# Performance work log

Measured on AMD Instinct MI355X. Metric: run time of the kernel, lower is better.

The kernel has to match this reference:

```python
import jax, jax.numpy as jnp
import numpy as np

B, C, H, W = 4, 256, 64, 64

def _conv1x1(x, w, b):
    # x: [B,C,H,W], w: [O,C] (1x1 conv kernel squeezed), b: [O]
    return jnp.einsum('bchw,oc->bohw', x, w) + b[None, :, None, None]

def setup_inputs() -> dict:
    key = jax.random.key(0)
    ks = jax.random.split(key, 9)
    s = 1.0 / np.sqrt(C)
    inp = {'x': jax.random.normal(ks[0], (B, C, H, W), dtype=jnp.float32)}
    for i, name in enumerate(['f', 'g', 'h', 'v']):
        inp['W' + name] = jax.random.uniform(ks[1 + 2 * i], (C, C), jnp.float32, -s, s)
        inp['b' + name] = jax.random.uniform(ks[2 + 2 * i], (C,), jnp.float32, -s, s)
    return inp

def reference(x, Wf, bf, Wg, bg, Wh, bh, Wv, bv):
    b, c, h, w = x.shape
    n = h * w
    f = _conv1x1(x, Wf, bf).reshape(b, c, n)  # [B,C,N]
    g = _conv1x1(x, Wg, bg).reshape(b, c, n)  # [B,C,N]
    hh = _conv1x1(x, Wh, bh).reshape(b, c, n)  # [B,C,N]
    fg = jnp.einsum('bci,bcj->bij', f, g)      # [B,N,N], no scaling (as in source)
    attn = jax.nn.softmax(fg, axis=1)          # softmax over dim=1 (first N axis)
    fgh = jnp.einsum('bci,bij->bcj', hh, attn) # [B,C,N]
    return _conv1x1(fgh.reshape(b, c, h, w), Wv, bv)
```

## Files before the change

kernel.cpp:

```cpp
#include <hip/hip_runtime.h>
#include <hip/hip_bf16.h>


typedef short short8 __attribute__((ext_vector_type(8)));
typedef short short4v __attribute__((ext_vector_type(4)));
typedef float f32x4 __attribute__((ext_vector_type(4)));
typedef _Float16 f16x8 __attribute__((ext_vector_type(8)));
typedef unsigned short u16;
typedef unsigned int u32;

#define DEV static __device__ __forceinline__
#define MFMA16(a, b, c) __builtin_amdgcn_mfma_f32_16x16x32_f16(a, b, c, 0, 0, 0)

DEV u16 h16(float x) {
    union { _Float16 h; u16 u; } c;
    c.h = (_Float16)x;
    return c.u;
}
DEV f16x8 ldh8(const u16* p) { return *reinterpret_cast<const f16x8*>(p); }

DEV u32 cvtpk(float a, float b) {
    u32 r;
    asm("v_cvt_pkrtz_f16_f32 %0, %1, %2" : "=v"(r) : "v"(a), "v"(b));
    return r;
}

DEV void gload16(const void* g, void* l) {
    __builtin_amdgcn_global_load_lds(
        (const __attribute__((address_space(1))) unsigned int*)g,
        (__attribute__((address_space(3))) unsigned int*)l, 16, 0, 0);
}

constexpr size_t OFF_WH = 0;
constexpr size_t OFF_WV = 131072;
constexpr size_t OFF_MB = 262144;
constexpr size_t OFF_ML = 266240;
constexpr size_t OFF_M  = 524288;
constexpr size_t OFF_U  = 1310720;
constexpr size_t OFF_H  = OFF_U + 8388608;
constexpr size_t OFF_XT = OFF_H + 8388608;
constexpr size_t OFF_OP = OFF_XT + 8388608;

__global__ __launch_bounds__(256) void k_gemm_M(
    const float* __restrict__ Wf, const float* __restrict__ Wg,
    const float* __restrict__ bg, const float* __restrict__ Wh,
    const float* __restrict__ Wv,
    u16* __restrict__ M, float* __restrict__ Mb, u16* WH, u16* WV) {
    int c = blockIdx.x;
    int t = threadIdx.x;
    size_t rowi = (size_t)c * 256 + t;
    WH[rowi] = h16(Wh[rowi]);
    WV[rowi] = h16(Wv[rowi]);
    __shared__ float wf[256];
    wf[t] = Wf[(size_t)t * 256 + c];
    __syncthreads();
    float acc = 0.f;
    for (int o = 0; o < 256; ++o) acc += wf[o] * Wg[(size_t)o * 256 + t];
    M[rowi] = h16(acc);
    if (t == 0) {
        float s = 0.f;
        for (int o = 0; o < 256; ++o) s += wf[o] * bg[o];
        Mb[c] = s;
    }
}

__global__ __launch_bounds__(256) void k_prep(
    const float* __restrict__ x, const u16* __restrict__ M,
    const float* __restrict__ Mb, const u16* __restrict__ WH,
    const float* __restrict__ bh,
    u16* __restrict__ Xt, u16* __restrict__ U, u16* __restrict__ Hb) {
    __shared__ float tbuf[64][65];
    __shared__ u16 xt[64][264];

    int bid = blockIdx.x;
    int m0 = bid * 64;
    int b = m0 >> 12, n0 = m0 & 4095;
    int tid = threadIdx.x;
    int tx = tid & 63, ty = tid >> 6;
    int nl = tid >> 2, cg = tid & 3;

    for (int ct4 = 0; ct4 < 4; ++ct4) {
        const float* src = x + ((size_t)(b * 256 + ct4 * 64)) * 4096 + n0;
#pragma unroll
        for (int k = 0; k < 16; ++k) {
            int cl = ty * 16 + k;
            tbuf[cl][tx] = src[(size_t)cl * 4096 + tx];
        }
        __syncthreads();
        short8 h0, h1;
#pragma unroll
        for (int j = 0; j < 8; ++j) h0[j] = (short)h16(tbuf[cg * 16 + j][nl]);
#pragma unroll
        for (int j = 8; j < 16; ++j) h1[j - 8] = (short)h16(tbuf[cg * 16 + j][nl]);
        int colbase = ct4 * 64 + cg * 16;
        *reinterpret_cast<short8*>(&xt[nl][colbase]) = h0;
        *reinterpret_cast<short8*>(&xt[nl][colbase + 8]) = h1;
        size_t dst = ((size_t)(m0 + nl)) * 256 + colbase;
        *reinterpret_cast<short8*>(Xt + dst) = h0;
        *reinterpret_cast<short8*>(Xt + dst + 8) = h1;
        __syncthreads();
    }

    int w = tid >> 6, lane = tid & 63, r = lane & 15, g = lane >> 4;
    f16x8 A[8];
#pragma unroll
    for (int ks = 0; ks < 8; ++ks)
        A[ks] = *reinterpret_cast<const f16x8*>(&xt[w * 16 + r][ks * 32 + 8 * g]);

#pragma unroll 4
    for (int ot = 0; ot < 16; ++ot) {
        f32x4 au = {0.f, 0.f, 0.f, 0.f};
        f32x4 ah = {0.f, 0.f, 0.f, 0.f};
        const u16* mrow = M + (size_t)(ot * 16 + r) * 256;
        const u16* hrow = WH + (size_t)(ot * 16 + r) * 256;
#pragma unroll
        for (int ks = 0; ks < 8; ++ks) {
            int k0 = ks * 32 + 8 * g;
            au = MFMA16(A[ks], ldh8(mrow + k0), au);
            ah = MFMA16(A[ks], ldh8(hrow + k0), ah);
        }
        int o = ot * 16 + r;
        float mb = Mb[o];
        float bhv = bh[o];
#pragma unroll
        for (int q = 0; q < 4; ++q) {
            int rloc = w * 16 + 4 * g + q;
            U[(size_t)(m0 + rloc) * 256 + o] = h16(au[q] + mb);
            int n = n0 + rloc;
            int k5 = n & 31;
            int kp = (k5 < 16) ? (8 * (k5 >> 2) + (k5 & 3))
                               : (8 * ((k5 - 16) >> 2) + 4 + (k5 & 3));
            int np = (n & ~31) | kp;
            Hb[((size_t)(b * 256 + o)) * 4096 + np] = h16(ah[q] + bhv);
        }
    }
}

__global__ __launch_bounds__(256, 2) void k_attn(
    const u16* __restrict__ F, const u16* __restrict__ G,
    const u16* __restrict__ Hb, u16* __restrict__ OP, float* __restrict__ ML) {
    __shared__ u16 Kd[2][8192];
    __shared__ u16 Vd[2][8192];

    int bid = blockIdx.x;
    int xcd = bid & 7, idx = bid >> 3;
    int b = xcd >> 1, ks = xcd & 1;
    int tid = threadIdx.x;
    int w = tid >> 6, lane = tid & 63, r = lane & 15, g = lane >> 4;
    int j0 = idx * 64 + w * 16;
    const float L2E = 1.4426950408889634f;

    int vlc = (r >> 1) * 128 + (((16 * g) + (r & 1) * 64) ^ (((r >> 1) & 7) << 4));

    f16x8 Qf[8];
    {
        const u16* q = G + (size_t)(b * 4096 + j0 + r) * 256;
#pragma unroll
        for (int k = 0; k < 8; ++k) Qf[k] = ldh8(q + k * 32 + 8 * g);
    }
    f32x4 O[16];
#pragma unroll
    for (int i = 0; i < 16; ++i) O[i] = {0.f, 0.f, 0.f, 0.f};
    float m = -1e30f, l = 0.f;

    const char* Fb  = (const char*)(F + (size_t)b * 4096 * 256);
    const char* Hbb = (const char*)(Hb + (size_t)b * 256 * 4096);

    int ksrc[4], vsrc[4];
#pragma unroll
    for (int t = 0; t < 4; ++t) {
        int d = (w * 4 + t) * 1024 + lane * 16;
        int row = d >> 9, col = d & 511;
        ksrc[t] = row * 512 + (col ^ ((row & 7) << 4));
        int r128 = d >> 7, wn = d & 127;
        int wp = wn ^ ((r128 & 7) << 4);
        vsrc[t] = ((r128 * 2 + (wp >> 6)) << 13) + (wp & 63);
    }

#define STAGE(bufn, I0)                                                         \
    do {                                                                        \
        const char* kb_ = Fb + (size_t)(I0) * 512;                              \
        const char* vb_ = Hbb + (size_t)(I0) * 2;                               \
        char* kl = (char*)Kd[bufn];                                             \
        char* vl = (char*)Vd[bufn];                                             \
        _Pragma("unroll") for (int t = 0; t < 4; ++t)                           \
            gload16(kb_ + ksrc[t], kl + (w * 4 + t) * 1024);                    \
        _Pragma("unroll") for (int t = 0; t < 4; ++t)                           \
            gload16(vb_ + vsrc[t], vl + (w * 4 + t) * 1024);                    \
    } while (0)

    int i0beg = ks * 2048;
    STAGE(0, i0beg);
    __syncthreads();

    for (int it = 0; it < 64; ++it) {
        int cur = it & 1;
        if (it + 1 < 64) STAGE(cur ^ 1, i0beg + (it + 1) * 32);

        const char* Kl = (const char*)Kd[cur];
        const char* Vb = (const char*)Vd[cur] + vlc;

        f32x4 s0 = {0.f, 0.f, 0.f, 0.f};
        f32x4 s1 = {0.f, 0.f, 0.f, 0.f};
        __builtin_amdgcn_s_setprio(1);
        {
            const char* kr = Kl + r * 512;
            int sw = (r & 7) << 4;
#pragma unroll
            for (int k = 0; k < 8; ++k) {
                f16x8 ka = *reinterpret_cast<const f16x8*>(kr + ((k * 64 + 16 * g) ^ sw));
                s0 = MFMA16(ka, Qf[k], s0);
            }
        }
        {
            const char* kr = Kl + (16 + r) * 512;
            int sw = (r & 7) << 4;
#pragma unroll
            for (int k = 0; k < 8; ++k) {
                f16x8 ka = *reinterpret_cast<const f16x8*>(kr + ((k * 64 + 16 * g) ^ sw));
                s1 = MFMA16(ka, Qf[k], s1);
            }
        }
        __builtin_amdgcn_s_setprio(0);

        float v = fmaxf(fmaxf(fmaxf(s0[0], s0[1]), fmaxf(s0[2], s0[3])),
                        fmaxf(fmaxf(s1[0], s1[1]), fmaxf(s1[2], s1[3])));
        if (!__all(v - m <= 8.0f)) {
            v = fmaxf(v, __shfl_xor(v, 16));
            v = fmaxf(v, __shfl_xor(v, 32));
            float mn = fmaxf(m, v);
            float corr = exp2f((m - mn) * L2E);
            m = mn;
            l *= corr;
#pragma unroll
            for (int ct = 0; ct < 16; ++ct) O[ct] *= corr;
        }
#pragma unroll
        for (int q = 0; q < 4; ++q) {
            s0[q] = exp2f((s0[q] - m) * L2E);
            s1[q] = exp2f((s1[q] - m) * L2E);
        }
        l += (s0[0] + s0[1] + s0[2] + s0[3]) + (s1[0] + s1[1] + s1[2] + s1[3]);

        union { u32 wd[4]; f16x8 fr; } pu;
        pu.wd[0] = cvtpk(s0[0], s0[1]);
        pu.wd[1] = cvtpk(s0[2], s0[3]);
        pu.wd[2] = cvtpk(s1[0], s1[1]);
        pu.wd[3] = cvtpk(s1[2], s1[3]);

        __builtin_amdgcn_s_setprio(1);
#pragma unroll
        for (int ct = 0; ct < 16; ++ct) {
            f16x8 vb = *reinterpret_cast<const f16x8*>(Vb + ct * 1024);
            O[ct] = MFMA16(vb, pu.fr, O[ct]);
        }
        __builtin_amdgcn_s_setprio(0);

        __syncthreads();
    }
#undef STAGE

    l += __shfl_xor(l, 16);
    l += __shfl_xor(l, 32);
    float inv = 1.f / l;
    size_t mrow = (size_t)ks * 16384 + b * 4096 + j0 + r;
#pragma unroll
    for (int ct = 0; ct < 16; ++ct) {
        short4v pk;
#pragma unroll
        for (int q = 0; q < 4; ++q) pk[q] = (short)h16(O[ct][q] * inv);
        *reinterpret_cast<short4v*>(OP + mrow * 256 + ct * 16 + 4 * g) = pk;
    }
    if (g == 0) {
        size_t mi = mrow * 2;
        ML[mi] = m;
        ML[mi + 1] = l;
    }
}

__global__ __launch_bounds__(256) void k_conv_out(
    const u16* __restrict__ WV, const u16* __restrict__ OP,
    const float* __restrict__ ML, const float* __restrict__ bv,
    float* __restrict__ out) {
    int bidn = blockIdx.x & 255, bido = blockIdx.x >> 8;
    int w = threadIdx.x >> 6, lane = threadIdx.x & 63, r = lane & 15, g = lane >> 4;
    int o0 = bido * 64 + w * 16, n0 = bidn * 64;
    const float L2E = 1.4426950408889634f;
    float wl0[4], wl1[4];
    int nfs[4];
#pragma unroll
    for (int ntl = 0; ntl < 4; ++ntl) {
        int nf = n0 + ntl * 16 + r;
        nfs[ntl] = nf;
        float m0_ = ML[(size_t)nf * 2], l0_ = ML[(size_t)nf * 2 + 1];
        float m1_ = ML[((size_t)16384 + nf) * 2], l1_ = ML[((size_t)16384 + nf) * 2 + 1];
        float M_ = fmaxf(m0_, m1_);
        float a0 = exp2f((m0_ - M_) * L2E) * l0_;
        float a1 = exp2f((m1_ - M_) * L2E) * l1_;
        float inv = 1.f / (a0 + a1);
        wl0[ntl] = a0 * inv;
        wl1[ntl] = a1 * inv;
    }
    f32x4 acc[4];
#pragma unroll
    for (int i = 0; i < 4; ++i) acc[i] = {0.f, 0.f, 0.f, 0.f};
    const u16* arow = WV + (size_t)(o0 + r) * 256;
#pragma unroll
    for (int ks = 0; ks < 8; ++ks) {
        int k0 = ks * 32 + 8 * g;
        f16x8 a = ldh8(arow + k0);
#pragma unroll
        for (int ntl = 0; ntl < 4; ++ntl) {
            f16x8 v0 = ldh8(OP + (size_t)nfs[ntl] * 256 + k0);
            f16x8 v1 = ldh8(OP + ((size_t)16384 + nfs[ntl]) * 256 + k0);
            union { u32 wd[4]; f16x8 fr; } bb;
#pragma unroll
            for (int j = 0; j < 4; ++j) {
                float e0 = wl0[ntl] * (float)v0[2 * j] + wl1[ntl] * (float)v1[2 * j];
                float e1 = wl0[ntl] * (float)v0[2 * j + 1] + wl1[ntl] * (float)v1[2 * j + 1];
                bb.wd[j] = cvtpk(e0, e1);
            }
            acc[ntl] = MFMA16(a, bb.fr, acc[ntl]);
        }
    }
#pragma unroll
    for (int ntl = 0; ntl < 4; ++ntl) {
#pragma unroll
        for (int q = 0; q < 4; ++q) {
            int o = o0 + 4 * g + q;
            int nf = nfs[ntl];
            int bb2 = nf >> 12, n = nf & 4095;
            out[((size_t)(bb2 * 256 + o)) * 4096 + n] = acc[ntl][q] + bv[o];
        }
    }
}

extern "C" void kernel_launch(void* const* d_in, const int* in_sizes, int n_in,
                              void* d_out, int out_size, void* d_ws, size_t ws_size,
                              hipStream_t stream) {
    const float* x  = (const float*)d_in[0];
    const float* Wf = (const float*)d_in[1];
    const float* bf = (const float*)d_in[2];
    const float* Wg = (const float*)d_in[3];
    const float* bg = (const float*)d_in[4];
    const float* Wh = (const float*)d_in[5];
    const float* bh = (const float*)d_in[6];
    const float* Wv = (const float*)d_in[7];
    const float* bv = (const float*)d_in[8];
    float* out = (float*)d_out;
    char* ws = (char*)d_ws;
    (void)bf;

    u16* WH = (u16*)(ws + OFF_WH);
    u16* WV = (u16*)(ws + OFF_WV);
    float* MB = (float*)(ws + OFF_MB);
    float* ML = (float*)(ws + OFF_ML);
    u16* M  = (u16*)(ws + OFF_M);
    u16* U  = (u16*)(ws + OFF_U);
    u16* H  = (u16*)(ws + OFF_H);
    u16* XT = (u16*)(ws + OFF_XT);
    u16* OP = (u16*)(ws + OFF_OP);

    k_gemm_M<<<256, 256, 0, stream>>>(Wf, Wg, bg, Wh, Wv, M, MB, WH, WV);
    k_prep<<<256, 256, 0, stream>>>(x, M, MB, WH, bh, XT, U, H);
    k_attn<<<512, 256, 0, stream>>>(XT, U, H, OP, ML);
    k_conv_out<<<1024, 256, 0, stream>>>(WV, OP, ML, bv, out);
}
```

Before: 204.5 us.

## Split attention key range four ways and add a separate merge kernel

The attention kernel now splits the key/value range into four partitions instead of two, so it launches twice as many blocks, each doing half as many iterations. The V tile is single-buffered, with an extra barrier inside each iteration to free LDS for higher occupancy, and the two-blocks-per-CU launch bound is dropped. A new merge kernel combines the four partial outputs with their max/sum statistics into a normalized fp16 buffer that reuses the U region. The output convolution becomes a plain GEMM on that buffer. The cost is twice the partial-output traffic, one more kernel launch and extra synchronization inside the loop.

After: 209.3 us. 2.4% more time.

```diff
diff --git a/kernel.cpp b/kernel.cpp
--- a/kernel.cpp
+++ b/kernel.cpp
@@ -35,11 +35,12 @@
 constexpr size_t OFF_WV = 131072;
 constexpr size_t OFF_MB = 262144;
 constexpr size_t OFF_ML = 266240;
-constexpr size_t OFF_M  = 524288;
+constexpr size_t OFF_M  = 790528;
 constexpr size_t OFF_U  = 1310720;
 constexpr size_t OFF_H  = OFF_U + 8388608;
 constexpr size_t OFF_XT = OFF_H + 8388608;
 constexpr size_t OFF_OP = OFF_XT + 8388608;
+constexpr size_t OFF_OT = OFF_U;
 
 __global__ __launch_bounds__(256) void k_gemm_M(
     const float* __restrict__ Wf, const float* __restrict__ Wg,
@@ -136,18 +137,20 @@
     }
 }
 
-__global__ __launch_bounds__(256, 2) void k_attn(
+__global__ __launch_bounds__(256) void k_attn(
     const u16* __restrict__ F, const u16* __restrict__ G,
     const u16* __restrict__ Hb, u16* __restrict__ OP, float* __restrict__ ML) {
     __shared__ u16 Kd[2][8192];
-    __shared__ u16 Vd[2][8192];
+    __shared__ u16 Vd[8192];
 
     int bid = blockIdx.x;
     int xcd = bid & 7, idx = bid >> 3;
-    int b = xcd >> 1, ks = xcd & 1;
+    int b = xcd >> 1;
+    int ks = ((idx & 1) << 1) | (xcd & 1);
+    int qb = idx >> 1;
     int tid = threadIdx.x;
     int w = tid >> 6, lane = tid & 63, r = lane & 15, g = lane >> 4;
-    int j0 = idx * 64 + w * 16;
+    int j0 = qb * 64 + w * 16;
     const float L2E = 1.4426950408889634f;
 
     int vlc = (r >> 1) * 128 + (((16 * g) + (r & 1) * 64) ^ (((r >> 1) & 7) << 4));
@@ -177,28 +180,32 @@
         vsrc[t] = ((r128 * 2 + (wp >> 6)) << 13) + (wp & 63);
     }
 
-#define STAGE(bufn, I0)                                                         \
+#define STAGE_K(bufn, I0)                                                       \
     do {                                                                        \
         const char* kb_ = Fb + (size_t)(I0) * 512;                              \
-        const char* vb_ = Hbb + (size_t)(I0) * 2;                               \
         char* kl = (char*)Kd[bufn];                                             \
-        char* vl = (char*)Vd[bufn];                                             \
         _Pragma("unroll") for (int t = 0; t < 4; ++t)                           \
             gload16(kb_ + ksrc[t], kl + (w * 4 + t) * 1024);                    \
+    } while (0)
+#define STAGE_V(I0)                                                             \
+    do {                                                                        \
+        const char* vb_ = Hbb + (size_t)(I0) * 2;                               \
+        char* vl = (char*)Vd;                                                   \
         _Pragma("unroll") for (int t = 0; t < 4; ++t)                           \
             gload16(vb_ + vsrc[t], vl + (w * 4 + t) * 1024);                    \
     } while (0)
 
-    int i0beg = ks * 2048;
-    STAGE(0, i0beg);
+    int i0beg = ks * 1024;
+    STAGE_K(0, i0beg);
+    STAGE_V(i0beg);
     __syncthreads();
 
-    for (int it = 0; it < 64; ++it) {
+    for (int it = 0; it < 32; ++it) {
         int cur = it & 1;
-        if (it + 1 < 64) STAGE(cur ^ 1, i0beg + (it + 1) * 32);
+        if (it > 0) STAGE_V(i0beg + it * 32);
+        if (it + 1 < 32) STAGE_K(cur ^ 1, i0beg + (it + 1) * 32);
 
         const char* Kl = (const char*)Kd[cur];
-        const char* Vb = (const char*)Vd[cur] + vlc;
 
         f32x4 s0 = {0.f, 0.f, 0.f, 0.f};
         f32x4 s1 = {0.f, 0.f, 0.f, 0.f};
@@ -248,6 +255,9 @@
         pu.wd[2] = cvtpk(s1[0], s1[1]);
         pu.wd[3] = cvtpk(s1[2], s1[3]);
 
+        __syncthreads();
+
+        const char* Vb = (const char*)Vd + vlc;
         __builtin_amdgcn_s_setprio(1);
 #pragma unroll
         for (int ct = 0; ct < 16; ++ct) {
@@ -258,7 +268,8 @@
 
         __syncthreads();
     }
-#undef STAGE
+#undef STAGE_K
+#undef STAGE_V
 
     l += __shfl_xor(l, 16);
     l += __shfl_xor(l, 32);
@@ -278,29 +289,49 @@
     }
 }
 
+__global__ __launch_bounds__(256) void k_merge(
+    const u16* __restrict__ OP, const float* __restrict__ ML, u16* __restrict__ OT) {
+    int t = blockIdx.x * 256 + threadIdx.x;
+    int m = t >> 5;
+    int c0 = (t & 31) * 8;
+    const float L2E = 1.4426950408889634f;
+    float mm[4], ll[4];
+    float M = -1e30f;
+#pragma unroll
+    for (int ks = 0; ks < 4; ++ks) {
+        size_t mi = ((size_t)ks * 16384 + m) * 2;
+        mm[ks] = ML[mi];
+        ll[ks] = ML[mi + 1];
+        M = fmaxf(M, mm[ks]);
+    }
+    float wl[4], L = 0.f;
+#pragma unroll
+    for (int ks = 0; ks < 4; ++ks) {
+        wl[ks] = exp2f((mm[ks] - M) * L2E) * ll[ks];
+        L += wl[ks];
+    }
+    float inv = 1.f / L;
+    float acc[8];
+#pragma unroll
+    for (int j = 0; j < 8; ++j) acc[j] = 0.f;
+#pragma unroll
+    for (int ks = 0; ks < 4; ++ks) {
+        f16x8 v = ldh8(OP + ((size_t)ks * 16384 + m) * 256 + c0);
+#pragma unroll
+        for (int j = 0; j < 8; ++j) acc[j] += wl[ks] * (float)v[j];
+    }
+    short8 outp;
+#pragma unroll
+    for (int j = 0; j < 8; ++j) outp[j] = (short)h16(acc[j] * inv);
+    *reinterpret_cast<short8*>(OT + (size_t)m * 256 + c0) = outp;
+}
+
 __global__ __launch_bounds__(256) void k_conv_out(
-    const u16* __restrict__ WV, const u16* __restrict__ OP,
-    const float* __restrict__ ML, const float* __restrict__ bv,
-    float* __restrict__ out) {
+    const u16* __restrict__ WV, const u16* __restrict__ OT,
+    const float* __restrict__ bv, float* __restrict__ out) {
     int bidn = blockIdx.x & 255, bido = blockIdx.x >> 8;
     int w = threadIdx.x >> 6, lane = threadIdx.x & 63, r = lane & 15, g = lane >> 4;
     int o0 = bido * 64 + w * 16, n0 = bidn * 64;
-    const float L2E = 1.4426950408889634f;
-    float wl0[4], wl1[4];
-    int nfs[4];
-#pragma unroll
-    for (int ntl = 0; ntl < 4; ++ntl) {
-        int nf = n0 + ntl * 16 + r;
-        nfs[ntl] = nf;
-        float m0_ = ML[(size_t)nf * 2], l0_ = ML[(size_t)nf * 2 + 1];
-        float m1_ = ML[((size_t)16384 + nf) * 2], l1_ = ML[((size_t)16384 + nf) * 2 + 1];
-        float M_ = fmaxf(m0_, m1_);
-        float a0 = exp2f((m0_ - M_) * L2E) * l0_;
-        float a1 = exp2f((m1_ - M_) * L2E) * l1_;
-        float inv = 1.f / (a0 + a1);
-        wl0[ntl] = a0 * inv;
-        wl1[ntl] = a1 * inv;
-    }
     f32x4 acc[4];
 #pragma unroll
     for (int i = 0; i < 4; ++i) acc[i] = {0.f, 0.f, 0.f, 0.f};
@@ -311,16 +342,8 @@
         f16x8 a = ldh8(arow + k0);
 #pragma unroll
         for (int ntl = 0; ntl < 4; ++ntl) {
-            f16x8 v0 = ldh8(OP + (size_t)nfs[ntl] * 256 + k0);
-            f16x8 v1 = ldh8(OP + ((size_t)16384 + nfs[ntl]) * 256 + k0);
-            union { u32 wd[4]; f16x8 fr; } bb;
-#pragma unroll
-            for (int j = 0; j < 4; ++j) {
-                float e0 = wl0[ntl] * (float)v0[2 * j] + wl1[ntl] * (float)v1[2 * j];
-                float e1 = wl0[ntl] * (float)v0[2 * j + 1] + wl1[ntl] * (float)v1[2 * j + 1];
-                bb.wd[j] = cvtpk(e0, e1);
-            }
-            acc[ntl] = MFMA16(a, bb.fr, acc[ntl]);
+            f16x8 bb = ldh8(OT + (size_t)(n0 + ntl * 16 + r) * 256 + k0);
+            acc[ntl] = MFMA16(a, bb, acc[ntl]);
         }
     }
 #pragma unroll
@@ -328,9 +351,9 @@
 #pragma unroll
         for (int q = 0; q < 4; ++q) {
             int o = o0 + 4 * g + q;
-            int nf = nfs[ntl];
-            int bb2 = nf >> 12, n = nf & 4095;
-            out[((size_t)(bb2 * 256 + o)) * 4096 + n] = acc[ntl][q] + bv[o];
+            int nf = n0 + ntl * 16 + r;
+            int bb = nf >> 12, n = nf & 4095;
+            out[((size_t)(bb * 256 + o)) * 4096 + n] = acc[ntl][q] + bv[o];
         }
     }
 }
@@ -360,9 +383,11 @@
     u16* H  = (u16*)(ws + OFF_H);
     u16* XT = (u16*)(ws + OFF_XT);
     u16* OP = (u16*)(ws + OFF_OP);
+    u16* OT = (u16*)(ws + OFF_OT);
 
     k_gemm_M<<<256, 256, 0, stream>>>(Wf, Wg, bg, Wh, Wv, M, MB, WH, WV);
     k_prep<<<256, 256, 0, stream>>>(x, M, MB, WH, bh, XT, U, H);
-    k_attn<<<512, 256, 0, stream>>>(XT, U, H, OP, ML);
-    k_conv_out<<<1024, 256, 0, stream>>>(WV, OP, ML, bv, out);
-}
+    k_attn<<<1024, 256, 0, stream>>>(XT, U, H, OP, ML);
+    k_merge<<<2048, 256, 0, stream>>>(OP, ML, OT);
+    k_conv_out<<<1024, 256, 0, stream>>>(WV, OT, bv, out);
+}
```
